# Kernel tuning notes

Hardware: AMD Instinct MI355X
Metric: run time of the kernel (lower is better)

The kernel has to match this reference:

```python
import jax, jax.numpy as jnp
import numpy as np

NUM_HEADS = 12
ACT_BITS = 8
W_BITS = 8
# I-BERT integer softmax constants (2nd-order polynomial approx of exp on (-ln2, 0])
EXP_COEF = (0.35815147, 0.96963238, 1.0)
LN2 = 0.6931471805599453
N_EXP = 30  # max number of ln2 shifts


def ste_round(x):
    # straight-through round
    return x + jax.lax.stop_gradient(jnp.round(x) - x)


def fq_act(x, bits=ACT_BITS):
    """Per-tensor asymmetric uint fake-quant (QAct). Returns (dequant, scale)."""
    mn = jax.lax.stop_gradient(jnp.min(x))
    mx = jax.lax.stop_gradient(jnp.max(x))
    qmax = 2.0 ** bits - 1.0
    scale = jnp.maximum((mx - mn) / qmax, 1e-8)
    zero = jnp.round(-mn / scale)
    q = jnp.clip(ste_round(x / scale) + zero, 0.0, qmax)
    return (q - zero) * scale, scale


def fq_weight(w, bits=W_BITS):
    """Per-output-channel symmetric int fake-quant (QuantLinear weight)."""
    amax = jax.lax.stop_gradient(jnp.max(jnp.abs(w), axis=1, keepdims=True))
    qmax = 2.0 ** (bits - 1) - 1.0
    scale = jnp.maximum(amax / qmax, 1e-8)
    q = jnp.clip(ste_round(w / scale), -qmax - 1.0, qmax)
    return q * scale


def int_softmax(x, scale):
    """I-BERT style integer softmax; `scale` is the quant scale of x."""
    a, b, c = EXP_COEF
    x_int = ste_round(x / scale)
    x_int = x_int - jnp.max(x_int, axis=-1, keepdims=True)  # <= 0
    x0_int = jnp.floor(-LN2 / scale)                         # negative integer
    x_int = jnp.maximum(x_int, N_EXP * x0_int)
    qexp = jnp.floor(x_int / x0_int)                         # >= 0 integer
    r = x_int - x0_int * qexp                                # residual in (x0_int, 0]
    b_int = jnp.floor(b / a / scale)
    c_int = jnp.floor(c / a / (scale * scale))
    p_int = r * (r + b_int) + c_int                          # int polynomial exp(r)
    e = p_int * jnp.exp2(-qexp) * (a * scale * scale)        # exp(x) approx
    return e / jnp.sum(e, axis=-1, keepdims=True)


def setup_inputs() -> dict:
    key = jax.random.key(0)
    ks = jax.random.split(key, 5)
    B, N, C = 64, 197, 768
    x = jax.random.normal(ks[0], (B, N, C), dtype=jnp.float32)
    w_qkv = jax.random.normal(ks[1], (3 * C, C), dtype=jnp.float32) * 0.02
    b_qkv = jax.random.normal(ks[2], (3 * C,), dtype=jnp.float32) * 0.02
    w_proj = jax.random.normal(ks[3], (C, C), dtype=jnp.float32) * 0.02
    b_proj = jax.random.normal(ks[4], (C,), dtype=jnp.float32) * 0.02
    return {"x": x, "w_qkv": w_qkv, "b_qkv": b_qkv, "w_proj": w_proj, "b_proj": b_proj}


def reference(x, w_qkv, b_qkv, w_proj, b_proj):
    B, N, C = x.shape
    H = NUM_HEADS
    D = C // H
    attn_scale = D ** -0.5

    # QuantLinear qkv: fake-quant weight, GEMM, fake-quant output
    qkv = jnp.einsum('bnc,oc->bno', x, fq_weight(w_qkv)) + b_qkv
    qkv, _ = fq_act(qkv)

    q, _ = fq_act(qkv[:, :, :C])          # attn_q_out
    k, _ = fq_act(qkv[:, :, C:2 * C])     # attn_k_out
    v, _ = fq_act(qkv[:, :, 2 * C:])      # attn_v_input

    q = q.reshape(B, N, H, D).transpose(0, 2, 1, 3)  # bhnd
    k = k.reshape(B, N, H, D).transpose(0, 2, 1, 3)
    v = v.reshape(B, N, H, D).transpose(0, 2, 1, 3)

    attn = jnp.einsum('bhnd,bhmd->bhnm', q, k) * attn_scale
    attn, kv_scale = fq_act(attn)          # attn_kv_out, provides scale to intSoft
    attn = int_softmax(attn, kv_scale)     # QuantIntSoft

    out = jnp.einsum('bhnm,bhmd->bhnd', attn, v)
    out = out.transpose(0, 2, 1, 3).reshape(B, N, C)
    out, _ = fq_act(out)                   # attn_v_out

    out = jnp.einsum('bnc,oc->bno', out, fq_weight(w_proj)) + b_proj
    out, _ = fq_act(out)                   # attn_proj output quant
    return out
```

## Files before the change

### kernel.cpp

```cpp
#include <hip/hip_runtime.h>


#define NB 64
#define NN 197
#define NC 768
#define NH 12
#define ND 64
#define NO3 2304
#define NBH (NB*NH)
#define NM (NB*NN)

typedef unsigned int u32;
typedef unsigned short u16;
typedef unsigned long long u64;
typedef short bf16x8 __attribute__((ext_vector_type(8)));
typedef float f32x4 __attribute__((ext_vector_type(4)));

__device__ __forceinline__ u32 fenc(float f){
  u32 u = __float_as_uint(f);
  return (u & 0x80000000u) ? ~u : (u | 0x80000000u);
}
__device__ __forceinline__ float fdec(u32 e){
  return (e & 0x80000000u) ? __uint_as_float(e ^ 0x80000000u) : __uint_as_float(~e);
}
__device__ __forceinline__ float wmin(float v){
#pragma unroll
  for (int o=32;o>0;o>>=1) v = fminf(v, __shfl_xor(v,o,64));
  return v;
}
__device__ __forceinline__ float wmax(float v){
#pragma unroll
  for (int o=32;o>0;o>>=1) v = fmaxf(v, __shfl_xor(v,o,64));
  return v;
}
__device__ __forceinline__ float fqdq(float x, float s, float z){
  float q = rintf(x/s) + z;
  q = fminf(fmaxf(q, 0.f), 255.f);
  return (q - z) * s;
}
__device__ __forceinline__ u16 tobf(float f){
  u32 u = __float_as_uint(f);
  return (u16)((u + 0x7fffu + ((u >> 16) & 1u)) >> 16);
}
__device__ __forceinline__ float frombf(u16 u){
  return __uint_as_float(((u32)u) << 16);
}
__device__ __forceinline__ void gload16(const void* g, void* l){
  __builtin_amdgcn_global_load_lds(
      (const __attribute__((address_space(1))) void*)g,
      (__attribute__((address_space(3))) void*)l, 16, 0, 0);
}

__device__ __forceinline__ void qkv_scales(const u32* slots, float* s2, float* z2,
                                           float* s1o, float* z1o){
  float mnr0=fdec(slots[0]), mxr0=fdec(slots[1]);
  float mnr1=fdec(slots[2]), mxr1=fdec(slots[3]);
  float mnr2=fdec(slots[4]), mxr2=fdec(slots[5]);
  float mn1 = fminf(mnr0, fminf(mnr1, mnr2));
  float mx1 = fmaxf(mxr0, fmaxf(mxr1, mxr2));
  float s1 = fmaxf((mx1-mn1)/255.0f, 1e-8f);
  float z1 = rintf(-mn1/s1);
  float a0 = fqdq(mnr0,s1,z1), b0 = fqdq(mxr0,s1,z1);
  float a1 = fqdq(mnr1,s1,z1), b1 = fqdq(mxr1,s1,z1);
  float a2 = fqdq(mnr2,s1,z1), b2 = fqdq(mxr2,s1,z1);
  s2[0] = fmaxf((b0-a0)/255.0f,1e-8f); z2[0] = rintf(-a0/s2[0]);
  s2[1] = fmaxf((b1-a1)/255.0f,1e-8f); z2[1] = rintf(-a1/s2[1]);
  s2[2] = fmaxf((b2-a2)/255.0f,1e-8f); z2[2] = rintf(-a2/s2[2]);
  *s1o = s1; *z1o = z1;
}

__global__ void k_init(u32* slots){
  int t = threadIdx.x;
  if (t < 12) slots[t] = (t & 1) ? 0u : 0xFFFFFFFFu;
}

__global__ __launch_bounds__(256) void k_wquant(const float* __restrict__ wqkv,
    const float* __restrict__ wproj, u16* __restrict__ B1, float* __restrict__ s1,
    u16* __restrict__ B2, float* __restrict__ s2){
  int row = blockIdx.x;
  const float* src; u16* dst; float* sd;
  if (row < NO3){ src = wqkv + (size_t)row*NC; dst = B1 + (size_t)row*NC; sd = s1 + row; }
  else { int r2 = row - NO3; src = wproj + (size_t)r2*NC; dst = B2 + (size_t)r2*NC; sd = s2 + r2; }
  int t = threadIdx.x;
  float w0 = src[t], w1 = src[t+256], w2 = src[t+512];
  float am = fmaxf(fabsf(w0), fmaxf(fabsf(w1), fabsf(w2)));
  __shared__ float red[4];
  am = wmax(am);
  if ((t&63)==0) red[t>>6] = am;
  __syncthreads();
  am = fmaxf(fmaxf(red[0],red[1]), fmaxf(red[2],red[3]));
  float s = fmaxf(am / 127.0f, 1e-8f);
  dst[t]     = tobf(fminf(fmaxf(rintf(w0/s), -128.f), 127.f));
  dst[t+256] = tobf(fminf(fmaxf(rintf(w1/s), -128.f), 127.f));
  dst[t+512] = tobf(fminf(fmaxf(rintf(w2/s), -128.f), 127.f));
  if (t==0) *sd = s;
}

__global__ __launch_bounds__(256) void k_xsplit(const float* __restrict__ x,
    u16* __restrict__ xhl){
  const u32 total = (u32)NM*192u;
  for (u32 i = blockIdx.x*256u + threadIdx.x; i < total; i += gridDim.x*256u){
    u32 row = i / 192u, kc = (i - row*192u)*4u;
    float4 v = *(const float4*)(x + (size_t)row*NC + kc);
    u16 h0=tobf(v.x), h1=tobf(v.y), h2=tobf(v.z), h3=tobf(v.w);
    u64 hp = (u64)h0 | ((u64)h1<<16) | ((u64)h2<<32) | ((u64)h3<<48);
    u64 lp = (u64)tobf(v.x-frombf(h0)) | ((u64)tobf(v.y-frombf(h1))<<16)
           | ((u64)tobf(v.z-frombf(h2))<<32) | ((u64)tobf(v.w-frombf(h3))<<48);
    size_t base = (size_t)row*1536 + kc;
    *(u64*)(xhl + base) = hp;
    *(u64*)(xhl + base + 768) = lp;
  }
}

__global__ __launch_bounds__(256) void k_transcode2(const float* __restrict__ p,
    u16* __restrict__ codes2, const u32* __restrict__ slots){
  float mn = fdec(slots[0]), mx = fdec(slots[1]);
  float s = fmaxf((mx-mn)/255.0f, 1e-8f);
  float z = rintf(-mn/s);
  const u32 total = (u32)NM*192u;
  for (u32 i = blockIdx.x*256u + threadIdx.x; i < total; i += gridDim.x*256u){
    u32 row = i / 192u, kc = (i - row*192u)*4u;
    float4 v = *(const float4*)(p + (size_t)row*NC + kc);
    u64 c0 = (u64)tobf(fminf(fmaxf(rintf(v.x/s)+z,0.f),255.f) - z);
    u64 c1 = (u64)tobf(fminf(fmaxf(rintf(v.y/s)+z,0.f),255.f) - z);
    u64 c2 = (u64)tobf(fminf(fmaxf(rintf(v.z/s)+z,0.f),255.f) - z);
    u64 c3 = (u64)tobf(fminf(fmaxf(rintf(v.w/s)+z,0.f),255.f) - z);
    *(u64*)(codes2 + (size_t)row*NC + kc) = c0 | (c1<<16) | (c2<<32) | (c3<<48);
  }
}

template<int MODE>
__global__ __launch_bounds__(256) void k_gemm_bf16(const u16* __restrict__ A, int KA,
    const u16* __restrict__ Bw, const float* __restrict__ sw,
    const float* __restrict__ bias, float* __restrict__ C, int O,
    const u32* __restrict__ qslot, u32* oslot)
{
  __shared__ u16 As[128*64];
  __shared__ u16 Bs[128*64];
  __shared__ float redn[4], redx[4];

  int tid = threadIdx.x;
  int l = tid & 63, w = tid >> 6;
  long m0 = (long)blockIdx.y * 128;
  long o0 = (long)blockIdx.x * 128;

  float sA = 1.f;
  if constexpr (MODE==1){
    float mn = fdec(qslot[0]), mx = fdec(qslot[1]);
    sA = fmaxf((mx-mn)/255.0f, 1e-8f);
  }

  int srow = tid >> 3;
  int scol = (tid & 7) * 8;
  long arow[4]; const u16* bpr[4];
#pragma unroll
  for (int q=0;q<4;q++){
    long mr = m0 + srow + q*32;
    arow[q] = (mr < NM) ? mr : (long)(NM-1);
    bpr[q] = Bw + (size_t)(o0 + srow + q*32) * NC + scol;
  }

  int wm = (w>>1)*64, wn = (w&1)*64;
  int fr = l & 15;
  int fcb = ((l>>4)*8)*2;

  f32x4 acc[4][4];
#pragma unroll
  for (int mi=0;mi<4;mi++)
#pragma unroll
    for (int ni=0;ni<4;ni++)
#pragma unroll
      for (int j=0;j<4;j++) acc[mi][ni][j] = 0.f;

  int nkt = KA >> 6;
  for (int kt=0; kt<nkt; kt++){
    int ka0 = kt*64;
    int kb0 = (ka0 >= NC) ? (ka0 - NC) : ka0;
    __syncthreads();
#pragma unroll
    for (int q=0;q<4;q++){
      gload16(A + (size_t)arow[q]*KA + ka0 + scol, &As[(srow + q*32)*64 + scol]);
      gload16(bpr[q] + kb0,                        &Bs[(srow + q*32)*64 + scol]);
    }
    __syncthreads();
#pragma unroll
    for (int ks=0; ks<2; ks++){
      bf16x8 bfr[4];
#pragma unroll
      for (int ni=0;ni<4;ni++)
        bfr[ni] = *(const bf16x8*)((const char*)&Bs[(wn + ni*16 + fr)*64] + ks*64 + fcb);
#pragma unroll
      for (int mi=0;mi<4;mi++){
        bf16x8 af = *(const bf16x8*)((const char*)&As[(wm + mi*16 + fr)*64] + ks*64 + fcb);
#pragma unroll
        for (int ni=0;ni<4;ni++)
          acc[mi][ni] = __builtin_amdgcn_mfma_f32_16x16x32_bf16(af, bfr[ni], acc[mi][ni], 0,0,0);
      }
    }
  }

  float cmn = 3.4e38f, cmx = -3.4e38f;
#pragma unroll
  for (int ni=0;ni<4;ni++){
    long col = o0 + wn + ni*16 + fr;
    float sc = sw[col];
    if constexpr (MODE==1) sc *= sA;
    float bb = bias[col];
#pragma unroll
    for (int mi=0;mi<4;mi++){
      long row0 = m0 + wm + mi*16 + (l>>4)*4;
#pragma unroll
      for (int j=0;j<4;j++){
        long rr = row0 + j;
        if (rr < NM){
          float v = acc[mi][ni][j] * sc + bb;
          C[rr*(long)O + col] = v;
          cmn = fminf(cmn, v); cmx = fmaxf(cmx, v);
        }
      }
    }
  }
  cmn = wmin(cmn); cmx = wmax(cmx);
  if (l==0){ redn[w] = cmn; redx[w] = cmx; }
  __syncthreads();
  if (tid==0){
    float mn = fminf(fminf(redn[0],redn[1]), fminf(redn[2],redn[3]));
    float mx = fmaxf(fmaxf(redx[0],redx[1]), fmaxf(redx[2],redx[3]));
    int sb = (MODE==0) ? 2*(int)(blockIdx.x/6) : 0;
    atomicMin(&oslot[sb],   fenc(mn));
    atomicMax(&oslot[sb+1], fenc(mx));
  }
}

__global__ __launch_bounds__(256) void k_transcode(const float* __restrict__ qkv,
    u16* __restrict__ codes, const u32* __restrict__ slots){
  float s2[3], z2[3], s1g, z1g;
  qkv_scales(slots, s2, z2, &s1g, &z1g);
  const u32 total = 3u*NBH*NN*16u;
  for (u32 i4 = blockIdx.x*256u + threadIdx.x; i4 < total; i4 += gridDim.x*256u){
    u32 d4 = i4 & 15u;
    u32 t1 = i4 >> 4;
    u32 n  = t1 % NN;
    u32 t2 = t1 / NN;
    u32 bh = t2 % NBH;
    u32 sl = t2 / NBH;
    u32 b = bh / NH, h = bh % NH;
    float4 v = *(const float4*)(qkv + ((size_t)b*NN + n)*NO3 + sl*NC + h*ND + d4*4u);
    float ss = s2[sl], zz = z2[sl];
    u64 c0 = (u64)tobf(fminf(fmaxf(rintf(fqdq(v.x,s1g,z1g)/ss)+zz,0.f),255.f) - zz);
    u64 c1 = (u64)tobf(fminf(fmaxf(rintf(fqdq(v.y,s1g,z1g)/ss)+zz,0.f),255.f) - zz);
    u64 c2 = (u64)tobf(fminf(fmaxf(rintf(fqdq(v.z,s1g,z1g)/ss)+zz,0.f),255.f) - zz);
    u64 c3 = (u64)tobf(fminf(fmaxf(rintf(fqdq(v.w,s1g,z1g)/ss)+zz,0.f),255.f) - zz);
    *(u64*)(codes + ((size_t)sl*NBH*NN + (size_t)bh*NN + n)*ND + d4*4u) =
        c0 | (c1<<16) | (c2<<32) | (c3<<48);
  }
}

template<int PASS>
__global__ __launch_bounds__(256) void k_attn(const u16* __restrict__ codes,
    float* __restrict__ rowmax, u32* slots, float* __restrict__ outp){
  __shared__ u16 Ks[64*72];
  __shared__ u16 Vt[(PASS==2)?64*72:8];
  __shared__ u16 EsH[(PASS==2)?64*72:8];
  __shared__ u16 EsL[(PASS==2)?64*72:8];
  __shared__ float redn[4], redx[4];

  const u16* qc = codes;
  const u16* kc = codes + (size_t)NBH*NN*ND;
  const u16* vc = codes + 2*(size_t)NBH*NN*ND;

  float s2[3], z2[3], s1g, z1g;
  qkv_scales(slots, s2, z2, &s1g, &z1g);
  float ss = 0.125f * s2[0] * s2[1];
  float sv = s2[2];

  float s=1.f, z=0.f, x0=-1.f, bint=0.f, cint=0.f, as2=0.f, x030=0.f;
  if constexpr (PASS==2){
    float mnA = fdec(slots[6]), mxA = fdec(slots[7]);
    s = fmaxf((mxA-mnA)/255.0f, 1e-8f);
    z = rintf(-mnA/s);
    x0 = floorf(-0.6931471805599453f / s);
    bint = floorf((float)(0.96963238/0.35815147) / s);
    cint = floorf((float)(1.0/0.35815147) / (s*s));
    as2 = (0.35815147f*s)*s;
    x030 = 30.f*x0;
  }

  int tid = threadIdx.x;
  int l = tid & 63, w = tid >> 6;
  int bh = blockIdx.y, nt = blockIdx.x;
  int lr = l & 15, lk = l >> 4;

  int qrow = nt*64 + w*16 + lr;
  bf16x8 aq0 = {}, aq1 = {};
  if (qrow < NN){
    const u16* qp = qc + ((size_t)bh*NN + qrow)*ND + lk*8;
    aq0 = *(const bf16x8*)qp;
    aq1 = *(const bf16x8*)(qp + 32);
  }

  int qr[4];
#pragma unroll
  for (int j=0;j<4;j++) qr[j] = nt*64 + w*16 + lk*4 + j;

  float rcode[4] = {0.f,0.f,0.f,0.f};
  if constexpr (PASS==2){
#pragma unroll
    for (int j=0;j<4;j++)
      if (qr[j] < NN)
        rcode[j] = fminf(fmaxf(rintf(rowmax[(size_t)bh*NN + qr[j]]/s)+z,0.f),255.f);
  }

  float gmn = 3.4e38f, gmx = -3.4e38f;
  float rmx[4] = {-3.4e38f,-3.4e38f,-3.4e38f,-3.4e38f};
  float den[4] = {0.f,0.f,0.f,0.f};
  f32x4 num[4];
#pragma unroll
  for (int dt=0;dt<4;dt++)
#pragma unroll
    for (int j=0;j<4;j++) num[dt][j] = 0.f;

  for (int mt=0; mt<4; mt++){
    __syncthreads();
#pragma unroll
    for (int rep=0; rep<2; rep++){
      int task = tid + rep*256;
      int row = task >> 3, dc = task & 7;
      int grow = mt*64 + row;
      bf16x8 kv8 = {};
      if (grow < NN) kv8 = *(const bf16x8*)(kc + ((size_t)bh*NN + grow)*ND + dc*8);
      *(bf16x8*)&Ks[row*72 + dc*8] = kv8;
      if constexpr (PASS==2){
        bf16x8 vv8 = {};
        if (grow < NN) vv8 = *(const bf16x8*)(vc + ((size_t)bh*NN + grow)*ND + dc*8);
#pragma unroll
        for (int jj=0;jj<8;jj++) Vt[(dc*8+jj)*72 + row] = (u16)vv8[jj];
      }
    }
    __syncthreads();

    f32x4 sca[4];
#pragma unroll
    for (int ct=0;ct<4;ct++)
#pragma unroll
      for (int j=0;j<4;j++) sca[ct][j] = 0.f;
#pragma unroll
    for (int ct=0;ct<4;ct++){
      bf16x8 bk0 = *(const bf16x8*)&Ks[(ct*16 + lr)*72 + lk*8];
      bf16x8 bk1 = *(const bf16x8*)&Ks[(ct*16 + lr)*72 + 32 + lk*8];
      sca[ct] = __builtin_amdgcn_mfma_f32_16x16x32_bf16(aq0, bk0, sca[ct], 0,0,0);
      sca[ct] = __builtin_amdgcn_mfma_f32_16x16x32_bf16(aq1, bk1, sca[ct], 0,0,0);
    }

    if constexpr (PASS==1){
#pragma unroll
      for (int ct=0;ct<4;ct++){
        int m = mt*64 + ct*16 + lr;
        bool mv = m < NN;
#pragma unroll
        for (int j=0;j<4;j++){
          float sc = sca[ct][j] * ss;
          if (mv && qr[j] < NN){
            gmn = fminf(gmn, sc); gmx = fmaxf(gmx, sc);
            rmx[j] = fmaxf(rmx[j], sc);
          }
        }
      }
    } else {
#pragma unroll
      for (int ct=0;ct<4;ct++){
        int m = mt*64 + ct*16 + lr;
        bool mv = m < NN;
#pragma unroll
        for (int j=0;j<4;j++){
          float e = 0.f;
          if (mv && qr[j] < NN){
            float sc = sca[ct][j] * ss;
            float code = fminf(fmaxf(rintf(sc/s)+z, 0.f), 255.f);
            float xx = fmaxf(code - rcode[j], x030);
            float qe = floorf(xx / x0);
            float rr = xx - x0*qe;
            float p = rr*(rr + bint) + cint;
            e = scalbnf(p, -(int)qe) * as2;
            den[j] += e;
          }
          u16 eh = tobf(e);
          int ea = (w*16 + lk*4 + j)*72 + ct*16 + lr;
          EsH[ea] = eh;
          EsL[ea] = tobf(e - frombf(eh));
        }
      }
      __syncthreads();
#pragma unroll
      for (int ks=0; ks<2; ks++){
        bf16x8 ahh = *(const bf16x8*)&EsH[(w*16 + lr)*72 + ks*32 + lk*8];
        bf16x8 ahl = *(const bf16x8*)&EsL[(w*16 + lr)*72 + ks*32 + lk*8];
#pragma unroll
        for (int dt=0; dt<4; dt++){
          bf16x8 bv = *(const bf16x8*)&Vt[(dt*16 + lr)*72 + ks*32 + lk*8];
          num[dt] = __builtin_amdgcn_mfma_f32_16x16x32_bf16(ahh, bv, num[dt], 0,0,0);
          num[dt] = __builtin_amdgcn_mfma_f32_16x16x32_bf16(ahl, bv, num[dt], 0,0,0);
        }
      }
    }
  }

  if constexpr (PASS==1){
#pragma unroll
    for (int j=0;j<4;j++){
#pragma unroll
      for (int o=1;o<16;o<<=1) rmx[j] = fmaxf(rmx[j], __shfl_xor(rmx[j], o, 64));
    }
    if (lr == 0){
#pragma unroll
      for (int j=0;j<4;j++)
        if (qr[j] < NN) rowmax[(size_t)bh*NN + qr[j]] = rmx[j];
    }
    gmn = wmin(gmn); gmx = wmax(gmx);
    if (l==0){ redn[w]=gmn; redx[w]=gmx; }
    __syncthreads();
    if (tid==0){
      float mn = fminf(fminf(redn[0],redn[1]), fminf(redn[2],redn[3]));
      float mx = fmaxf(fmaxf(redx[0],redx[1]), fmaxf(redx[2],redx[3]));
      atomicMin(&slots[6], fenc(mn));
      atomicMax(&slots[7], fenc(mx));
    }
  } else {
#pragma unroll
    for (int j=0;j<4;j++){
#pragma unroll
      for (int o=1;o<16;o<<=1) den[j] += __shfl_xor(den[j], o, 64);
    }
    int b = bh/NH, h = bh - b*NH;
    float gmn2 = 3.4e38f, gmx2 = -3.4e38f;
#pragma unroll
    for (int dt=0;dt<4;dt++){
#pragma unroll
      for (int j=0;j<4;j++){
        if (qr[j] < NN){
          float oo = num[dt][j] * sv / den[j];
          outp[((size_t)b*NN + qr[j])*NC + h*ND + dt*16 + lr] = oo;
          gmn2 = fminf(gmn2, oo); gmx2 = fmaxf(gmx2, oo);
        }
      }
    }
    gmn2 = wmin(gmn2); gmx2 = wmax(gmx2);
    if (l==0){ redn[w]=gmn2; redx[w]=gmx2; }
    __syncthreads();
    if (tid==0){
      float mn = fminf(fminf(redn[0],redn[1]), fminf(redn[2],redn[3]));
      float mx = fmaxf(fmaxf(redx[0],redx[1]), fmaxf(redx[2],redx[3]));
      atomicMin(&slots[8], fenc(mn));
      atomicMax(&slots[9], fenc(mx));
    }
  }
}

__global__ __launch_bounds__(256) void k_fq_inplace(float* x, long n4, const u32* __restrict__ slots){
  float mn = fdec(slots[0]), mx = fdec(slots[1]);
  float s = fmaxf((mx-mn)/255.0f, 1e-8f);
  float z = rintf(-mn/s);
  for (long i = (long)blockIdx.x*blockDim.x + threadIdx.x; i < n4; i += (long)gridDim.x*blockDim.x){
    float4 v = ((float4*)x)[i];
    v.x = fqdq(v.x,s,z); v.y = fqdq(v.y,s,z); v.z = fqdq(v.z,s,z); v.w = fqdq(v.w,s,z);
    ((float4*)x)[i] = v;
  }
}

extern "C" void kernel_launch(void* const* d_in, const int* in_sizes, int n_in,
                              void* d_out, int out_size, void* d_ws, size_t ws_size,
                              hipStream_t stream) {
  (void)in_sizes; (void)n_in; (void)out_size; (void)ws_size;
  const float* x      = (const float*)d_in[0];
  const float* w_qkv  = (const float*)d_in[1];
  const float* b_qkv  = (const float*)d_in[2];
  const float* w_proj = (const float*)d_in[3];
  const float* b_proj = (const float*)d_in[4];
  float* out = (float*)d_out;

  u32*   slots  = (u32*)d_ws;
  u16*   B1     = (u16*)((char*)d_ws + 256);
  u16*   B2     = B1 + (size_t)NO3*NC;
  float* s1     = (float*)(B2 + (size_t)NC*NC);
  float* s2     = s1 + NO3;
  float* rowmax = s2 + NC;
  float* qkv    = rowmax + (size_t)NBH*NN;
  u16*   codesR = (u16*)(qkv + (size_t)NM*NO3);
  u16*   xhl    = codesR;
  u16*   codes  = codesR;
  u16*   codes2 = codesR;
  float* outpv  = qkv;

  k_init<<<1, 64, 0, stream>>>(slots);
  k_wquant<<<NO3 + NC, 256, 0, stream>>>(w_qkv, w_proj, B1, s1, B2, s2);
  k_xsplit<<<1024, 256, 0, stream>>>(x, xhl);
  k_gemm_bf16<0><<<dim3(NO3/128, 99), 256, 0, stream>>>(xhl, 1536, B1, s1, b_qkv, qkv, NO3, nullptr, slots);
  k_transcode<<<2048, 256, 0, stream>>>(qkv, codes, slots);
  k_attn<1><<<dim3(4, NBH), 256, 0, stream>>>(codes, rowmax, slots, nullptr);
  k_attn<2><<<dim3(4, NBH), 256, 0, stream>>>(codes, rowmax, slots, outpv);
  k_transcode2<<<1024, 256, 0, stream>>>(outpv, codes2, slots + 8);
  k_gemm_bf16<1><<<dim3(NC/128, 99), 256, 0, stream>>>(codes2, 768, B2, s2, b_proj, out, NC, slots + 8, slots + 10);
  k_fq_inplace<<<1024, 256, 0, stream>>>(out, (long)NM*NC/4, slots + 10);
}
```

Before: 551.3 us.

## Double-buffer GEMM LDS tiles with prefetch and XOR-swizzled layout

The bf16 MFMA GEMM now keeps two LDS buffers and issues the global-to-LDS loads for the next K tile before computing the current one, waiting with a partial vmcnt so memory latency overlaps the MFMA work. The LDS layout is also XOR-swizzled by row on the global source side, so fragment reads hit different banks. In exchange LDS use doubles to 64KB per block, which may reduce occupancy, and correctness now depends on hand-written waitcnt and barrier placement.

```diff
diff --git a/kernel.cpp b/kernel.cpp
--- a/kernel.cpp
+++ b/kernel.cpp
@@ -49,6 +49,16 @@
   __builtin_amdgcn_global_load_lds(
       (const __attribute__((address_space(1))) void*)g,
       (__attribute__((address_space(3))) void*)l, 16, 0, 0);
+}
+__device__ __forceinline__ void pipe_fence(){
+  __builtin_amdgcn_sched_barrier(0);
+}
+__device__ __forceinline__ void pipe_barrier(){
+  __builtin_amdgcn_sched_barrier(0);
+  asm volatile("" ::: "memory");
+  __builtin_amdgcn_s_barrier();
+  asm volatile("" ::: "memory");
+  __builtin_amdgcn_sched_barrier(0);
 }
 
 __device__ __forceinline__ void qkv_scales(const u32* slots, float* s2, float* z2,
@@ -135,8 +145,7 @@
     const float* __restrict__ bias, float* __restrict__ C, int O,
     const u32* __restrict__ qslot, u32* oslot)
 {
-  __shared__ u16 As[128*64];
-  __shared__ u16 Bs[128*64];
+  __shared__ u16 Ls[2][2][128*64];
   __shared__ float redn[4], redx[4];
 
   int tid = threadIdx.x;
@@ -151,18 +160,21 @@
   }
 
   int srow = tid >> 3;
-  int scol = (tid & 7) * 8;
-  long arow[4]; const u16* bpr[4];
+  int sch  = tid & 7;
+  int sof  = sch * 8;
+  int sx   = (sch ^ (srow & 7)) * 8;
+  long arow[4]; long brow[4];
 #pragma unroll
   for (int q=0;q<4;q++){
     long mr = m0 + srow + q*32;
     arow[q] = (mr < NM) ? mr : (long)(NM-1);
-    bpr[q] = Bw + (size_t)(o0 + srow + q*32) * NC + scol;
+    brow[q] = o0 + srow + q*32;
   }
 
   int wm = (w>>1)*64, wn = (w&1)*64;
   int fr = l & 15;
-  int fcb = ((l>>4)*8)*2;
+  int c4 = l >> 4;
+  int fx = fr & 7;
 
   f32x4 acc[4][4];
 #pragma unroll
@@ -173,30 +185,46 @@
       for (int j=0;j<4;j++) acc[mi][ni][j] = 0.f;
 
   int nkt = KA >> 6;
+#pragma unroll
+  for (int q=0;q<4;q++){
+    gload16(A  + (size_t)arow[q]*KA + sx, &Ls[0][0][(srow+q*32)*64 + sof]);
+    gload16(Bw + (size_t)brow[q]*NC + sx, &Ls[0][1][(srow+q*32)*64 + sof]);
+  }
+
   for (int kt=0; kt<nkt; kt++){
-    int ka0 = kt*64;
-    int kb0 = (ka0 >= NC) ? (ka0 - NC) : ka0;
-    __syncthreads();
-#pragma unroll
-    for (int q=0;q<4;q++){
-      gload16(A + (size_t)arow[q]*KA + ka0 + scol, &As[(srow + q*32)*64 + scol]);
-      gload16(bpr[q] + kb0,                        &Bs[(srow + q*32)*64 + scol]);
-    }
-    __syncthreads();
+    int cur = kt & 1;
+    if (kt+1 < nkt){
+      int ka0 = (kt+1)*64;
+      int kb0 = (ka0 >= NC) ? (ka0 - NC) : ka0;
+      int nb = cur ^ 1;
+#pragma unroll
+      for (int q=0;q<4;q++){
+        gload16(A  + (size_t)arow[q]*KA + ka0 + sx, &Ls[nb][0][(srow+q*32)*64 + sof]);
+        gload16(Bw + (size_t)brow[q]*NC + kb0 + sx, &Ls[nb][1][(srow+q*32)*64 + sof]);
+      }
+      asm volatile("s_waitcnt vmcnt(8)" ::: "memory");
+    } else {
+      asm volatile("s_waitcnt vmcnt(0)" ::: "memory");
+    }
+    pipe_barrier();
+    const u16* Ab = &Ls[cur][0][0];
+    const u16* Bb = &Ls[cur][1][0];
 #pragma unroll
     for (int ks=0; ks<2; ks++){
+      int co = (((ks<<2) | c4) ^ fx) * 8;
       bf16x8 bfr[4];
 #pragma unroll
       for (int ni=0;ni<4;ni++)
-        bfr[ni] = *(const bf16x8*)((const char*)&Bs[(wn + ni*16 + fr)*64] + ks*64 + fcb);
+        bfr[ni] = *(const bf16x8*)&Bb[(wn + ni*16 + fr)*64 + co];
 #pragma unroll
       for (int mi=0;mi<4;mi++){
-        bf16x8 af = *(const bf16x8*)((const char*)&As[(wm + mi*16 + fr)*64] + ks*64 + fcb);
+        bf16x8 af = *(const bf16x8*)&Ab[(wm + mi*16 + fr)*64 + co];
 #pragma unroll
         for (int ni=0;ni<4;ni++)
           acc[mi][ni] = __builtin_amdgcn_mfma_f32_16x16x32_bf16(af, bfr[ni], acc[mi][ni], 0,0,0);
       }
     }
+    pipe_barrier();
   }
 
   float cmn = 3.4e38f, cmx = -3.4e38f;
```

After: 562.5 us. 1.02x slower.
